# Kernel tuning notes

Hardware: AMD Instinct MI355X
Metric: run time of the kernel (lower is better)

Reference implementation:

```python
import jax, jax.numpy as jnp
import numpy as np
from jax.scipy.linalg import expm

D = 512      # d_model
S = 3        # num_scales
BATCH = 256
H = 8        # attention heads
HD = D // H  # head dim


def layernorm(x, g, b, eps=1e-5):
    m = jnp.mean(x, axis=-1, keepdims=True)
    v = jnp.var(x, axis=-1, keepdims=True)
    return (x - m) / jnp.sqrt(v + eps) * g + b


def setup_inputs() -> dict:
    key = jax.random.key(0)
    ks = jax.random.split(key, 16)
    sd = 1.0 / np.sqrt(D)
    inp = {
        'x': jax.random.normal(ks[0], (BATCH, D), jnp.float32),
        'h_prev': jax.random.normal(ks[1], (BATCH, D), jnp.float32),
        'lstm_h': jax.random.normal(ks[2], (S, BATCH, D), jnp.float32) * 0.1,
        'lstm_c': jax.random.normal(ks[3], (S, BATCH, D), jnp.float32) * 0.1,
        'A': jax.random.normal(ks[4], (D, D), jnp.float32) * sd,
        'Bm': jax.random.normal(ks[5], (D, D), jnp.float32) * sd,
        'dn_w1': jax.random.normal(ks[6], (D, D), jnp.float32) * sd,
        'dn_b1': jnp.zeros((D,), jnp.float32),
        'dn_g': jnp.ones((D,), jnp.float32),
        'dn_beta': jnp.zeros((D,), jnp.float32),
        'dn_w2': jax.random.normal(ks[7], (1, D), jnp.float32) * sd,
        'dn_b2': jnp.zeros((1,), jnp.float32),
        'lstm_wih': jax.random.normal(ks[8], (S, 4 * D, D), jnp.float32) * sd,
        'lstm_whh': jax.random.normal(ks[9], (S, 4 * D, D), jnp.float32) * sd,
        'lstm_bih': jnp.zeros((S, 4 * D), jnp.float32),
        'lstm_bhh': jnp.zeros((S, 4 * D), jnp.float32),
        'decays': jnp.linspace(0.5, 0.95, S, dtype=jnp.float32),
        'attn_in_w': jax.random.normal(ks[10], (3 * D, D), jnp.float32) * sd,
        'attn_in_b': jnp.zeros((3 * D,), jnp.float32),
        'attn_out_w': jax.random.normal(ks[11], (D, D), jnp.float32) * sd,
        'attn_out_b': jnp.zeros((D,), jnp.float32),
        'proj_w': jax.random.normal(ks[12], (D, (S + 2) * D), jnp.float32) * (1.0 / np.sqrt((S + 2) * D)),
        'proj_b': jnp.zeros((D,), jnp.float32),
        'proj_g': jnp.ones((D,), jnp.float32),
        'proj_beta': jnp.zeros((D,), jnp.float32),
    }
    return inp


def reference(x, h_prev, lstm_h, lstm_c, A, Bm, dn_w1, dn_b1, dn_g, dn_beta,
              dn_w2, dn_b2, lstm_wih, lstm_whh, lstm_bih, lstm_bhh, decays,
              attn_in_w, attn_in_b, attn_out_w, attn_out_b,
              proj_w, proj_b, proj_g, proj_beta):
    # ---- delta_net: Linear -> LayerNorm -> GELU(exact) -> Linear -> Softplus ----
    h1 = layernorm(x @ dn_w1.T + dn_b1, dn_g, dn_beta)
    h1 = jax.nn.gelu(h1, approximate=False)
    delta = jax.nn.softplus(h1 @ dn_w2.T + dn_b2)           # (B, 1)

    # ---- SSM update: h_t = expm(delta*A) h_prev + delta*B x ----
    A_disc = jax.vmap(expm)(delta[:, :, None] * A)          # (B, D, D)
    h_ssm = jnp.einsum('bij,bj->bi', A_disc, h_prev) + delta * jnp.einsum('ij,bj->bi', Bm, x)

    # ---- multi-scale LSTM cells (vectorized over scales) ----
    gates = (jnp.einsum('bd,skd->sbk', x, lstm_wih)
             + jnp.einsum('sbd,skd->sbk', lstm_h, lstm_whh)
             + (lstm_bih + lstm_bhh)[:, None, :])           # (S, B, 4D)
    gi, gf, gg, go = jnp.split(gates, 4, axis=-1)
    i_g = jax.nn.sigmoid(gi)
    f_g = jax.nn.sigmoid(gf)
    g_g = jnp.tanh(gg)
    o_g = jax.nn.sigmoid(go)
    c_raw = f_g * lstm_c + i_g * g_g                        # (S, B, D)
    h_new = o_g * jnp.tanh(c_raw)                           # (S, B, D)
    dec = decays[:, None, None]
    c_new = dec * lstm_c + (1.0 - dec) * c_raw              # (S, B, D)

    # ---- fusion attention: 1 query (h_ssm), S keys/values (h_new) ----
    Wq, Wk, Wv = jnp.split(attn_in_w, 3, axis=0)
    bq, bk, bv = jnp.split(attn_in_b, 3, axis=0)
    kv = jnp.transpose(h_new, (1, 0, 2))                    # (B, S, D)
    q = (h_ssm @ Wq.T + bq).reshape(-1, 1, H, HD).transpose(0, 2, 1, 3)   # (B,H,1,HD)
    k = (kv @ Wk.T + bk).reshape(-1, S, H, HD).transpose(0, 2, 1, 3)      # (B,H,S,HD)
    v = (kv @ Wv.T + bv).reshape(-1, S, H, HD).transpose(0, 2, 1, 3)
    scores = jnp.einsum('bhqe,bhke->bhqk', q, k) / np.sqrt(HD)
    attn = jax.nn.softmax(scores, axis=-1)
    ctx = jnp.einsum('bhqk,bhke->bhqe', attn, v)            # (B,H,1,HD)
    ctx = ctx.transpose(0, 2, 1, 3).reshape(-1, D)          # (B, D)
    fused = ctx @ attn_out_w.T + attn_out_b                 # (B, D)

    # ---- output projection over concat [h_ssm, fused, h_1..h_S] ----
    combined = jnp.concatenate([h_ssm, fused] + [h_new[i] for i in range(S)], axis=-1)
    output = layernorm(combined @ proj_w.T + proj_b, proj_g, proj_beta)
    return (output, h_ssm, h_new, c_new)
```

## Files before the change

### kernel.cpp

```cpp
#include <hip/hip_runtime.h>
#include <math.h>

#define DIM 512
#define NB 256
#define KMAX 12

using bf16x8 = __attribute__((ext_vector_type(8))) short;
using f32x4  = __attribute__((ext_vector_type(4))) float;
using float4v = __attribute__((ext_vector_type(4))) float;
using ushort4v = __attribute__((ext_vector_type(4))) unsigned short;

__device__ __forceinline__ unsigned short f2b(float f) {
    union { float f; unsigned int u; } v; v.f = f;
    unsigned int r = v.u + 0x7fffu + ((v.u >> 16) & 1u);
    return (unsigned short)(r >> 16);
}
__device__ __forceinline__ float b2f(unsigned short u) {
    union { unsigned int u; float f; } v; v.u = ((unsigned int)u) << 16;
    return v.f;
}
__device__ __forceinline__ ushort4v f2b4(float4v v) {
    ushort4v o;
    o.x = f2b(v.x); o.y = f2b(v.y); o.z = f2b(v.z); o.w = f2b(v.w);
    return o;
}

__device__ __forceinline__ void block_reduce2(float& s, float& q, float* sb1, float* sb2)
{
    int tid = threadIdx.x;
    #pragma unroll
    for (int off = 32; off > 0; off >>= 1) {
        s += __shfl_down(s, off);
        q += __shfl_down(q, off);
    }
    if ((tid & 63) == 0) { sb1[tid >> 6] = s; sb2[tid >> 6] = q; }
    __syncthreads();
    s = sb1[0] + sb1[1] + sb1[2] + sb1[3];
    q = sb2[0] + sb2[1] + sb2[2] + sb2[3];
    __syncthreads();
}

struct GemmDesc {
    const unsigned short* X;
    const unsigned short* W;
    const float* bias;
    float* Cf;
    unsigned short* Cb;
    unsigned short* Ct;
    int M, N, K, ldX, ldW, ldC, tr_row0, acc;
};
struct GemmArgs { GemmDesc d[10]; };
struct LnParams {
    const float* pre; const float* g; const float* beta;
    const float* w2; const float* b2; float* delta; float* coeff;
    int lnd_y;
};

__global__ __launch_bounds__(256) void gemm_mfma(GemmArgs args, LnParams lp)
{
    __shared__ unsigned short lsA[2][8192];
    __shared__ unsigned short lsB[2][8192];
    __shared__ float sb1[4], sb2[4];

    if ((int)blockIdx.y == lp.lnd_y) {
        int b = blockIdx.x, tid = threadIdx.x;
        int i0 = tid, i1 = tid + 256;
        float x0 = lp.pre[(size_t)b * DIM + i0];
        float x1 = lp.pre[(size_t)b * DIM + i1];
        float s = x0 + x1, q = x0 * x0 + x1 * x1;
        block_reduce2(s, q, sb1, sb2);
        float mean = s * (1.f / DIM);
        float var  = q * (1.f / DIM) - mean * mean;
        float inv  = rsqrtf(var + 1e-5f);
        float y0 = (x0 - mean) * inv * lp.g[i0] + lp.beta[i0];
        float y1 = (x1 - mean) * inv * lp.g[i1] + lp.beta[i1];
        float h0 = 0.5f * y0 * (1.f + erff(y0 * 0.70710678118654752f));
        float h1 = 0.5f * y1 * (1.f + erff(y1 * 0.70710678118654752f));
        float p = h0 * lp.w2[i0] + h1 * lp.w2[i1];
        float dummy = 0.f;
        block_reduce2(p, dummy, sb1, sb2);
        if (tid == 0) {
            float z = p + lp.b2[0];
            float d = (z > 20.f) ? z : log1pf(expf(z));
            lp.delta[b] = d;
            float c = 1.f;
            lp.coeff[b] = 1.f;
            for (int k = 1; k <= KMAX; ++k) { c *= d / (float)k; lp.coeff[k * 256 + b] = c; }
        }
        return;
    }

    GemmDesc de = args.d[blockIdx.y];
    int tn = de.N >> 6;
    int tiles = (de.M >> 6) * tn;
    int t = blockIdx.x;
    if (t >= tiles) return;
    int m0 = (t / tn) << 6;
    int n0 = (t % tn) << 6;

    int tid = threadIdx.x;
    int w = tid >> 6;
    int l = tid & 63;
    int nkt = de.K >> 7;

    int srow = w * 16 + (l >> 2);
    int schk = l & 3;
    const unsigned short* gA = de.X + (size_t)(m0 + srow) * de.ldX + schk * 8;
    const unsigned short* gB = de.W + (size_t)(n0 + srow) * de.ldW + schk * 8;
    unsigned short* lA = &lsA[0][(w * 64 + l) * 8];
    unsigned short* lB = &lsB[0][(w * 64 + l) * 8];

#define STAGE(bufi, kt)                                                          \
    do {                                                                         \
        for (int hh = 0; hh < 4; ++hh) {                                         \
            __builtin_amdgcn_global_load_lds(                                    \
                (const __attribute__((address_space(1))) unsigned int*)(gA + (size_t)(kt) * 128 + hh * 32), \
                (__attribute__((address_space(3))) unsigned int*)(lA + (bufi) * 8192 + hh * 2048), 16, 0, 0); \
            __builtin_amdgcn_global_load_lds(                                    \
                (const __attribute__((address_space(1))) unsigned int*)(gB + (size_t)(kt) * 128 + hh * 32), \
                (__attribute__((address_space(3))) unsigned int*)(lB + (bufi) * 8192 + hh * 2048), 16, 0, 0); \
        }                                                                        \
    } while (0)

    int mbase = (w >> 1) * 32;
    int nbase = (w & 1) * 32;

    f32x4 acc[2][2];
    #pragma unroll
    for (int i = 0; i < 2; ++i)
        #pragma unroll
        for (int j = 0; j < 2; ++j)
            acc[i][j] = (f32x4){0.f, 0.f, 0.f, 0.f};

    int kg = l >> 4;
    int fr = l & 15;
    int aslot = (mbase * 4 + fr * 4 + kg) * 8;
    int bslot = (nbase * 4 + fr * 4 + kg) * 8;

    STAGE(0, 0);

    for (int kt = 0; kt < nkt; ++kt) {
        __syncthreads();
        if (kt + 1 < nkt) STAGE((kt + 1) & 1, kt + 1);

        const unsigned short* bufA = &lsA[kt & 1][0];
        const unsigned short* bufB = &lsB[kt & 1][0];
        #pragma unroll
        for (int h = 0; h < 4; ++h) {
            bf16x8 a0 = *(const bf16x8*)(bufA + h * 2048 + aslot);
            bf16x8 a1 = *(const bf16x8*)(bufA + h * 2048 + aslot + 512);
            bf16x8 b0 = *(const bf16x8*)(bufB + h * 2048 + bslot);
            bf16x8 b1 = *(const bf16x8*)(bufB + h * 2048 + bslot + 512);
            acc[0][0] = __builtin_amdgcn_mfma_f32_16x16x32_bf16(a0, b0, acc[0][0], 0, 0, 0);
            acc[0][1] = __builtin_amdgcn_mfma_f32_16x16x32_bf16(a0, b1, acc[0][1], 0, 0, 0);
            acc[1][0] = __builtin_amdgcn_mfma_f32_16x16x32_bf16(a1, b0, acc[1][0], 0, 0, 0);
            acc[1][1] = __builtin_amdgcn_mfma_f32_16x16x32_bf16(a1, b1, acc[1][1], 0, 0, 0);
        }
    }

    #pragma unroll
    for (int mi = 0; mi < 2; ++mi) {
        #pragma unroll
        for (int ni = 0; ni < 2; ++ni) {
            int col = n0 + nbase + ni * 16 + fr;
            float bv = de.bias ? de.bias[col] : 0.f;
            #pragma unroll
            for (int r = 0; r < 4; ++r) {
                int row = m0 + mbase + mi * 16 + (l >> 4) * 4 + r;
                float v = acc[mi][ni][r] + bv;
                if (de.Cf) {
                    if (de.acc == 2)      atomicAdd(&de.Cf[(size_t)row * de.ldC + col], v);
                    else if (de.acc == 1) de.Cf[(size_t)row * de.ldC + col] += v;
                    else                  de.Cf[(size_t)row * de.ldC + col] = v;
                } else {
                    de.Cb[(size_t)row * de.ldC + col] = f2b(v);
                }
                if (de.Ct && row >= de.tr_row0)
                    de.Ct[(size_t)col * 512 + (row - de.tr_row0)] = f2b(v);
            }
        }
    }
#undef STAGE
}

#define NSEG 14
struct PrepArgs {
    const float* sA[NSEG]; const float* sB[NSEG]; unsigned short* dst[NSEG];
    int n4[NSEG], dRL4[NSEG], sRLA4[NSEG], sRLB4[NSEG], half4[NSEG], offA[NSEG];
    const float* A; unsigned short* ATb;
    float* gates_zero; int gz_n4;
};
__global__ __launch_bounds__(256) void prep_kernel(PrepArgs a)
{
    __shared__ float tile[32][33];
    int bid = blockIdx.x, tid = threadIdx.x;
    if (bid < 2048) {
        const int gstride = 2048 * 256;
        int g0 = bid * 256 + tid;
        for (int seg = 0; seg < NSEG; ++seg) {
            int n4 = a.n4[seg];
            const float* sA = a.sA[seg];
            const float* sB = a.sB[seg];
            unsigned short* d = a.dst[seg];
            int dRL4 = a.dRL4[seg], sRLA4 = a.sRLA4[seg], sRLB4 = a.sRLB4[seg];
            int half4 = a.half4[seg], offA = a.offA[seg];
            for (int i = g0; i < n4; i += gstride) {
                int r = i / dRL4, c = i - r * dRL4;
                const float* src = (c < half4)
                    ? sA + ((size_t)r * sRLA4 + offA + c) * 4
                    : sB + ((size_t)r * sRLB4 + (c - half4)) * 4;
                float4v v = *(const float4v*)src;
                *(ushort4v*)(d + (size_t)i * 4) = f2b4(v);
            }
        }
    } else if (bid < 2304) {
        int tt = bid - 2048;
        int bx = tt & 15, by = tt >> 4;
        int tx = tid & 31, ty = tid >> 5;
        #pragma unroll
        for (int i = 0; i < 32; i += 8)
            tile[ty + i][tx] = a.A[(size_t)(by * 32 + ty + i) * 512 + bx * 32 + tx];
        __syncthreads();
        #pragma unroll
        for (int i = 0; i < 32; i += 8)
            a.ATb[(size_t)(bx * 32 + ty + i) * 512 + by * 32 + tx] = f2b(tile[tx][ty + i]);
    } else {
        float4v* gz = (float4v*)a.gates_zero;
        int g0 = (bid - 2304) * 256 + tid;
        const int gstride = 128 * 256;
        float4v z = (float4v){0.f, 0.f, 0.f, 0.f};
        for (int i = g0; i < a.gz_n4; i += gstride) gz[i] = z;
    }
}

__global__ void pointwise_fused(
    const float* __restrict__ Tm, const float* __restrict__ coeff,
    const float* __restrict__ h_prev, const float* __restrict__ delta,
    const float* __restrict__ Bx, float* __restrict__ hssm,
    unsigned short* __restrict__ combb,
    const float* __restrict__ gates, const float* __restrict__ bih,
    const float* __restrict__ bhh, const float* __restrict__ cin,
    const float* __restrict__ decays,
    float* __restrict__ hout, float* __restrict__ cout,
    const float* __restrict__ proj_b, float* __restrict__ projout)
{
    int idx4 = blockIdx.x * 256 + threadIdx.x;
    int base = idx4 * 4;
    if (base < 131072) {
        int b = base >> 9, i = base & 511;
        const float* Tr = Tm + (size_t)b * (KMAX * DIM) + i;
        float4v a = *(const float4v*)(h_prev + base);
        #pragma unroll
        for (int k = 1; k <= KMAX; ++k) {
            float c = coeff[k * 256 + b];
            float4v t = *(const float4v*)(Tr + (size_t)(k - 1) * DIM);
            a.x += c * t.x; a.y += c * t.y; a.z += c * t.z; a.w += c * t.w;
        }
        float dl = delta[b];
        float4v bx = *(const float4v*)(Bx + base);
        a.x += dl * bx.x; a.y += dl * bx.y; a.z += dl * bx.z; a.w += dl * bx.w;
        *(float4v*)(hssm + base) = a;
        *(ushort4v*)(combb + (size_t)b * 2048 + i) = f2b4(a);
    } else if (base < 524288) {
        int i2 = base - 131072;
        int s = i2 / (NB * DIM);
        int r = i2 - s * (NB * DIM);
        int b = r >> 9, d = r & 511;
        const float* gr = gates + (size_t)s * 524288 + (size_t)b * 2048 + d;
        const float* bi = bih + s * 2048 + d;
        const float* bh = bhh + s * 2048 + d;
        float4v gi = *(const float4v*)(gr);
        float4v gf = *(const float4v*)(gr + 512);
        float4v gg = *(const float4v*)(gr + 1024);
        float4v go = *(const float4v*)(gr + 1536);
        float4v bi0 = *(const float4v*)(bi),        bh0 = *(const float4v*)(bh);
        float4v bi1 = *(const float4v*)(bi + 512),  bh1 = *(const float4v*)(bh + 512);
        float4v bi2 = *(const float4v*)(bi + 1024), bh2 = *(const float4v*)(bh + 1024);
        float4v bi3 = *(const float4v*)(bi + 1536), bh3 = *(const float4v*)(bh + 1536);
        float4v c = *(const float4v*)(cin + i2);
        float dec = decays[s];
        float4v hn, cn;
        #pragma unroll
        for (int j = 0; j < 4; ++j) {
            float vgi = ((const float*)&gi)[j] + ((const float*)&bi0)[j] + ((const float*)&bh0)[j];
            float vgf = ((const float*)&gf)[j] + ((const float*)&bi1)[j] + ((const float*)&bh1)[j];
            float vgg = ((const float*)&gg)[j] + ((const float*)&bi2)[j] + ((const float*)&bh2)[j];
            float vgo = ((const float*)&go)[j] + ((const float*)&bi3)[j] + ((const float*)&bh3)[j];
            float ig = 1.f / (1.f + expf(-vgi));
            float fg = 1.f / (1.f + expf(-vgf));
            float g_ = tanhf(vgg);
            float og = 1.f / (1.f + expf(-vgo));
            float cc = ((const float*)&c)[j];
            float craw = fg * cc + ig * g_;
            ((float*)&hn)[j] = og * tanhf(craw);
            ((float*)&cn)[j] = dec * cc + (1.f - dec) * craw;
        }
        *(float4v*)(hout + i2) = hn;
        *(float4v*)(cout + i2) = cn;
        *(ushort4v*)(combb + (size_t)b * 2048 + 512 + s * 512 + d) = f2b4(hn);
    } else {
        int i = idx4 - 131072;
        int c4 = i & 127;
        float4v pb = *(const float4v*)(proj_b + c4 * 4);
        *(float4v*)(projout + (size_t)i * 4) = pb;
    }
}

__global__ __launch_bounds__(256) void tail_kernel(
    const unsigned short* __restrict__ qb, const unsigned short* __restrict__ kvb,
    const unsigned short* __restrict__ aout_wb, const float* __restrict__ aout_b,
    const unsigned short* __restrict__ P2b, const float* __restrict__ projA,
    const float* __restrict__ fin_g, const float* __restrict__ fin_beta,
    float* __restrict__ outp)
{
    __shared__ float ctxs[512];
    __shared__ float fusedl[512];
    __shared__ float totals[512];
    __shared__ float sb1[4], sb2[4];
    int b = blockIdx.x, tid = threadIdx.x;

    if (tid < 128) {
        int h = tid >> 4, sub = (tid & 15) * 4;
        int col = h * 64 + sub;
        ushort4v q4 = *(const ushort4v*)(qb + (size_t)b * 512 + col);
        float qf[4] = { b2f(q4.x), b2f(q4.y), b2f(q4.z), b2f(q4.w) };
        float p[3];
        ushort4v k4[3], v4[3];
        #pragma unroll
        for (int s = 0; s < 3; ++s) {
            k4[s] = *(const ushort4v*)(kvb + (size_t)s * 262144 + (size_t)b * 1024 + col);
            v4[s] = *(const ushort4v*)(kvb + (size_t)s * 262144 + (size_t)b * 1024 + 512 + col);
            p[s] = qf[0] * b2f(k4[s].x) + qf[1] * b2f(k4[s].y)
                 + qf[2] * b2f(k4[s].z) + qf[3] * b2f(k4[s].w);
        }
        #pragma unroll
        for (int off = 1; off < 16; off <<= 1) {
            p[0] += __shfl_xor(p[0], off);
            p[1] += __shfl_xor(p[1], off);
            p[2] += __shfl_xor(p[2], off);
        }
        const float scale = 0.125f;
        float p0 = p[0] * scale, p1 = p[1] * scale, p2 = p[2] * scale;
        float m = fmaxf(p0, fmaxf(p1, p2));
        float w0 = expf(p0 - m), w1 = expf(p1 - m), w2 = expf(p2 - m);
        float invs = 1.f / (w0 + w1 + w2);
        ctxs[col + 0] = (w0 * b2f(v4[0].x) + w1 * b2f(v4[1].x) + w2 * b2f(v4[2].x)) * invs;
        ctxs[col + 1] = (w0 * b2f(v4[0].y) + w1 * b2f(v4[1].y) + w2 * b2f(v4[2].y)) * invs;
        ctxs[col + 2] = (w0 * b2f(v4[0].z) + w1 * b2f(v4[1].z) + w2 * b2f(v4[2].z)) * invs;
        ctxs[col + 3] = (w0 * b2f(v4[0].w) + w1 * b2f(v4[1].w) + w2 * b2f(v4[2].w)) * invs;
    }
    __syncthreads();

    for (int jj = tid; jj < 512; jj += 256) {
        float acc = aout_b[jj];
        const unsigned short* wr = aout_wb + (size_t)jj * 512;
        for (int k = 0; k < 512; k += 8) {
            ushort4v w0 = *(const ushort4v*)(wr + k);
            ushort4v w1 = *(const ushort4v*)(wr + k + 4);
            acc += ctxs[k+0]*b2f(w0.x) + ctxs[k+1]*b2f(w0.y)
                 + ctxs[k+2]*b2f(w0.z) + ctxs[k+3]*b2f(w0.w)
                 + ctxs[k+4]*b2f(w1.x) + ctxs[k+5]*b2f(w1.y)
                 + ctxs[k+6]*b2f(w1.z) + ctxs[k+7]*b2f(w1.w);
        }
        fusedl[jj] = acc;
    }
    __syncthreads();

    for (int ii = tid; ii < 512; ii += 256) {
        float acc = projA[(size_t)b * 512 + ii];
        const unsigned short* pr = P2b + (size_t)ii * 512;
        for (int j = 0; j < 512; j += 8) {
            ushort4v w0 = *(const ushort4v*)(pr + j);
            ushort4v w1 = *(const ushort4v*)(pr + j + 4);
            acc += fusedl[j+0]*b2f(w0.x) + fusedl[j+1]*b2f(w0.y)
                 + fusedl[j+2]*b2f(w0.z) + fusedl[j+3]*b2f(w0.w)
                 + fusedl[j+4]*b2f(w1.x) + fusedl[j+5]*b2f(w1.y)
                 + fusedl[j+6]*b2f(w1.z) + fusedl[j+7]*b2f(w1.w);
        }
        totals[ii] = acc;
    }
    __syncthreads();

    float x0 = totals[tid], x1 = totals[tid + 256];
    float s = x0 + x1, q = x0 * x0 + x1 * x1;
    block_reduce2(s, q, sb1, sb2);
    float mean = s * (1.f / DIM);
    float var  = q * (1.f / DIM) - mean * mean;
    float inv  = rsqrtf(var + 1e-5f);
    outp[(size_t)b * DIM + tid]       = (x0 - mean) * inv * fin_g[tid]       + fin_beta[tid];
    outp[(size_t)b * DIM + tid + 256] = (x1 - mean) * inv * fin_g[tid + 256] + fin_beta[tid + 256];
}

extern "C" void kernel_launch(void* const* d_in, const int* in_sizes, int n_in,
                              void* d_out, int out_size, void* d_ws, size_t ws_size,
                              hipStream_t stream)
{
    const float* x        = (const float*)d_in[0];
    const float* h_prev   = (const float*)d_in[1];
    const float* lstm_h   = (const float*)d_in[2];
    const float* lstm_c   = (const float*)d_in[3];
    const float* A        = (const float*)d_in[4];
    const float* Bm       = (const float*)d_in[5];
    const float* dn_w1    = (const float*)d_in[6];
    const float* dn_b1    = (const float*)d_in[7];
    const float* dn_g     = (const float*)d_in[8];
    const float* dn_beta  = (const float*)d_in[9];
    const float* dn_w2    = (const float*)d_in[10];
    const float* dn_b2    = (const float*)d_in[11];
    const float* wih      = (const float*)d_in[12];
    const float* whh      = (const float*)d_in[13];
    const float* bih      = (const float*)d_in[14];
    const float* bhh      = (const float*)d_in[15];
    const float* decays   = (const float*)d_in[16];
    const float* ain_w    = (const float*)d_in[17];
    const float* ain_b    = (const float*)d_in[18];
    const float* aout_w   = (const float*)d_in[19];
    const float* aout_b   = (const float*)d_in[20];
    const float* proj_w   = (const float*)d_in[21];
    const float* proj_b   = (const float*)d_in[22];
    const float* proj_g   = (const float*)d_in[23];
    const float* proj_bt  = (const float*)d_in[24];

    float* out  = (float*)d_out;
    float* hssm = out + 131072;
    float* hnew = out + 262144;
    float* cnew = out + 655360;

    unsigned short* us = (unsigned short*)d_ws;
    unsigned short* hpb     = us;
    unsigned short* ATb     = us + 131072;
    unsigned short* dn_w1b  = us + 393216;
    unsigned short* Bmb     = us + 655360;
    unsigned short* ain_wb  = us + 917504;
    unsigned short* proj_wb = us + 1703936;
    unsigned short* P2b     = us + 2752512;
    unsigned short* aout_wb = us + 3014656;
    unsigned short* Pw      = us + 3276800;
    unsigned short* Qa      = us + 5373952;
    unsigned short* Qb      = us + 5636096;
    unsigned short* Wcat    = us + 5898240;
    unsigned short* Xcat    = us + 12189696;
    unsigned short* combb   = us + 12976128;
    unsigned short* qb      = us + 13500416;
    unsigned short* kvb     = us + 13631488;
    unsigned short* U8b     = us + 14417920;
    float* fbase  = (float*)(us + 14548992);
    float* pre1   = fbase;
    float* delta  = fbase + 131072;
    float* coeff  = fbase + 131328;
    float* Bx     = fbase + 134656;
    float* Tm     = fbase + 265728;
    float* gates  = fbase + 1838592;
    float* projout = pre1;

    LnParams lpOff; lpOff.pre = nullptr; lpOff.g = nullptr; lpOff.beta = nullptr;
    lpOff.w2 = nullptr; lpOff.b2 = nullptr; lpOff.delta = nullptr; lpOff.coeff = nullptr;
    lpOff.lnd_y = -1;

    PrepArgs pa;
    int sidx = 0;
    auto LIN = [&](const float* s, unsigned short* d, int n4) {
        pa.sA[sidx]=s; pa.sB[sidx]=s; pa.dst[sidx]=d; pa.n4[sidx]=n4;
        pa.dRL4[sidx]=n4; pa.sRLA4[sidx]=0; pa.sRLB4[sidx]=0;
        pa.half4[sidx]=n4; pa.offA[sidx]=0; ++sidx;
    };
    LIN(h_prev, hpb,     32768);
    LIN(A,      Pw,      65536);
    LIN(dn_w1,  dn_w1b,  65536);
    LIN(Bm,     Bmb,     65536);
    LIN(ain_w,  ain_wb,  196608);
    LIN(aout_w, aout_wb, 65536);
    pa.sA[sidx]=proj_w; pa.sB[sidx]=proj_w + 1024; pa.dst[sidx]=proj_wb; pa.n4[sidx]=262144;
    pa.dRL4[sidx]=512; pa.sRLA4[sidx]=640; pa.sRLB4[sidx]=640; pa.half4[sidx]=128; pa.offA[sidx]=0; ++sidx;
    pa.sA[sidx]=proj_w; pa.sB[sidx]=proj_w; pa.dst[sidx]=P2b; pa.n4[sidx]=65536;
    pa.dRL4[sidx]=128; pa.sRLA4[sidx]=640; pa.sRLB4[sidx]=640; pa.half4[sidx]=128; pa.offA[sidx]=128; ++sidx;
    for (int s = 0; s < 3; ++s) {
        pa.sA[sidx]=wih + (size_t)s*1048576; pa.sB[sidx]=whh + (size_t)s*1048576;
        pa.dst[sidx]=Wcat + (size_t)s*2097152; pa.n4[sidx]=524288;
        pa.dRL4[sidx]=256; pa.sRLA4[sidx]=128; pa.sRLB4[sidx]=128; pa.half4[sidx]=128; pa.offA[sidx]=0; ++sidx;
    }
    for (int s = 0; s < 3; ++s) {
        pa.sA[sidx]=x; pa.sB[sidx]=lstm_h + (size_t)s*131072;
        pa.dst[sidx]=Xcat + (size_t)s*262144; pa.n4[sidx]=65536;
        pa.dRL4[sidx]=256; pa.sRLA4[sidx]=128; pa.sRLB4[sidx]=128; pa.half4[sidx]=128; pa.offA[sidx]=0; ++sidx;
    }
    pa.A = A; pa.ATb = ATb;
    pa.gates_zero = gates; pa.gz_n4 = 393216;
    prep_kernel<<<2432, 256, 0, stream>>>(pa);

    GemmArgs ga;
    ga.d[0] = { Xcat, dn_w1b, dn_b1, pre1, nullptr, nullptr, 256, 512, 512, 1024, 512, 512, 0, 0 };
    ga.d[1] = { Xcat, Bmb,    nullptr, Bx,  nullptr, nullptr, 256, 512, 512, 1024, 512, 512, 0, 0 };
    ga.d[2] = { Pw, ATb, nullptr, nullptr, Pw + 1*262144, Qa, 512, 512, 512, 512, 512, 512, 0, 0 };
    for (int s = 0; s < 3; ++s)
        for (int half = 0; half < 2; ++half)
            ga.d[3 + s * 2 + half] = { Xcat + (size_t)s * 262144 + half * 512,
                                       Wcat + (size_t)s * 2097152 + half * 512, nullptr,
                                       gates + (size_t)s * 524288, nullptr, nullptr,
                                       256, 2048, 512, 1024, 1024, 2048, 0, 2 };
    gemm_mfma<<<dim3(128, 9), 256, 0, stream>>>(ga, lpOff);

    LnParams lp1 = { pre1, dn_g, dn_beta, dn_w2, dn_b2, delta, coeff, 1 };
    ga.d[0] = { Pw, Qa, nullptr, nullptr, Pw + 2*262144, Qb, 1024, 512, 512, 512, 512, 512, 512, 0 };
    gemm_mfma<<<dim3(256, 2), 256, 0, stream>>>(ga, lp1);

    ga.d[0] = { Pw, Qb, nullptr, nullptr, Pw + 4*262144, nullptr, 2048, 512, 512, 512, 512, 512, 0, 0 };
    gemm_mfma<<<dim3(256, 1), 256, 0, stream>>>(ga, lpOff);

    ga.d[0] = { hpb, Pw, nullptr, Tm, nullptr, nullptr, 256, 4096, 512, 512, 512, 6144, 0, 0 };
    ga.d[1] = { hpb, Pw + 7*262144, nullptr, nullptr, U8b, nullptr, 256, 512, 512, 512, 512, 512, 0, 0 };
    gemm_mfma<<<dim3(256, 2), 256, 0, stream>>>(ga, lpOff);

    ga.d[0] = { U8b, Pw, nullptr, Tm + 4096, nullptr, nullptr, 256, 2048, 512, 512, 512, 6144, 0, 0 };
    gemm_mfma<<<dim3(128, 1), 256, 0, stream>>>(ga, lpOff);

    pointwise_fused<<<640, 256, 0, stream>>>(Tm, coeff, h_prev, delta, Bx, hssm, combb,
                                             gates, bih, bhh, lstm_c, decays, hnew, cnew,
                                             proj_b, projout);

    ga.d[0] = { combb, ain_wb, ain_b, nullptr, qb, nullptr, 256, 512, 512, 2048, 512, 512, 0, 0 };
    for (int s = 0; s < 3; ++s)
        ga.d[1 + s] = { combb + 512 + (size_t)s * 512, ain_wb + 262144, ain_b + 512,
                        nullptr, kvb + (size_t)s * 262144, nullptr, 256, 1024, 512, 2048, 512, 1024, 0, 0 };
    for (int ks = 0; ks < 4; ++ks)
        ga.d[4 + ks] = { combb + ks * 512, proj_wb + ks * 512, nullptr, projout, nullptr, nullptr,
                         256, 512, 512, 2048, 2048, 512, 0, 2 };
    gemm_mfma<<<dim3(64, 8), 256, 0, stream>>>(ga, lpOff);

    tail_kernel<<<256, 256, 0, stream>>>(qb, kvb, aout_wb, aout_b, P2b, projout,
                                         proj_g, proj_bt, out);
}
```

Measured before the change: 232.1 us.

## Fold attention out-projection into output projection and drop split-K atomics

```diff
diff --git a/kernel.cpp b/kernel.cpp
--- a/kernel.cpp
+++ b/kernel.cpp
@@ -183,12 +183,12 @@
 #undef STAGE
 }
 
-#define NSEG 14
+#define NSEG 13
 struct PrepArgs {
     const float* sA[NSEG]; const float* sB[NSEG]; unsigned short* dst[NSEG];
     int n4[NSEG], dRL4[NSEG], sRLA4[NSEG], sRLB4[NSEG], half4[NSEG], offA[NSEG];
     const float* A; unsigned short* ATb;
-    float* gates_zero; int gz_n4;
+    const float* W2src; unsigned short* W2dst;
 };
 __global__ __launch_bounds__(256) void prep_kernel(PrepArgs a)
 {
@@ -213,23 +213,20 @@
                 *(ushort4v*)(d + (size_t)i * 4) = f2b4(v);
             }
         }
-    } else if (bid < 2304) {
+    } else {
         int tt = bid - 2048;
+        const float* src = a.A;
+        unsigned short* dst = a.ATb;
+        if (tt >= 256) { tt -= 256; src = a.W2src; dst = a.W2dst; }
         int bx = tt & 15, by = tt >> 4;
         int tx = tid & 31, ty = tid >> 5;
         #pragma unroll
         for (int i = 0; i < 32; i += 8)
-            tile[ty + i][tx] = a.A[(size_t)(by * 32 + ty + i) * 512 + bx * 32 + tx];
+            tile[ty + i][tx] = src[(size_t)(by * 32 + ty + i) * 512 + bx * 32 + tx];
         __syncthreads();
         #pragma unroll
         for (int i = 0; i < 32; i += 8)
-            a.ATb[(size_t)(bx * 32 + ty + i) * 512 + by * 32 + tx] = f2b(tile[tx][ty + i]);
-    } else {
-        float4v* gz = (float4v*)a.gates_zero;
-        int g0 = (bid - 2304) * 256 + tid;
-        const int gstride = 128 * 256;
-        float4v z = (float4v){0.f, 0.f, 0.f, 0.f};
-        for (int i = g0; i < a.gz_n4; i += gstride) gz[i] = z;
+            dst[(size_t)(bx * 32 + ty + i) * 512 + by * 32 + tx] = f2b(tile[tx][ty + i]);
     }
 }
 
@@ -242,7 +239,8 @@
     const float* __restrict__ bhh, const float* __restrict__ cin,
     const float* __restrict__ decays,
     float* __restrict__ hout, float* __restrict__ cout,
-    const float* __restrict__ proj_b, float* __restrict__ projout)
+    const unsigned short* __restrict__ P2b, const float* __restrict__ aout_b,
+    const float* __restrict__ proj_b, float* __restrict__ pbc)
 {
     int idx4 = blockIdx.x * 256 + threadIdx.x;
     int base = idx4 * 4;
@@ -299,23 +297,30 @@
         *(float4v*)(cout + i2) = cn;
         *(ushort4v*)(combb + (size_t)b * 2048 + 512 + s * 512 + d) = f2b4(hn);
     } else {
-        int i = idx4 - 131072;
-        int c4 = i & 127;
-        float4v pb = *(const float4v*)(proj_b + c4 * 4);
-        *(float4v*)(projout + (size_t)i * 4) = pb;
+        int ii = idx4 - 131072;
+        const unsigned short* pr = P2b + (size_t)ii * 512;
+        float acc = 0.f;
+        for (int k = 0; k < 512; k += 8) {
+            ushort4v w0 = *(const ushort4v*)(pr + k);
+            ushort4v w1 = *(const ushort4v*)(pr + k + 4);
+            float4v a0 = *(const float4v*)(aout_b + k);
+            float4v a1 = *(const float4v*)(aout_b + k + 4);
+            acc += a0.x * b2f(w0.x) + a0.y * b2f(w0.y)
+                 + a0.z * b2f(w0.z) + a0.w * b2f(w0.w)
+                 + a1.x * b2f(w1.x) + a1.y * b2f(w1.y)
+                 + a1.z * b2f(w1.z) + a1.w * b2f(w1.w);
+        }
+        pbc[ii] = proj_b[ii] + acc;
     }
 }
 
 __global__ __launch_bounds__(256) void tail_kernel(
     const unsigned short* __restrict__ qb, const unsigned short* __restrict__ kvb,
-    const unsigned short* __restrict__ aout_wb, const float* __restrict__ aout_b,
-    const unsigned short* __restrict__ P2b, const float* __restrict__ projA,
+    const unsigned short* __restrict__ M2b, const float* __restrict__ projA,
     const float* __restrict__ fin_g, const float* __restrict__ fin_beta,
     float* __restrict__ outp)
 {
     __shared__ float ctxs[512];
-    __shared__ float fusedl[512];
-    __shared__ float totals[512];
     __shared__ float sb1[4], sb2[4];
     int b = blockIdx.x, tid = threadIdx.x;
 
@@ -351,37 +356,25 @@
     }
     __syncthreads();
 
-    for (int jj = tid; jj < 512; jj += 256) {
-        float acc = aout_b[jj];
-        const unsigned short* wr = aout_wb + (size_t)jj * 512;
+    float x0 = projA[(size_t)b * 512 + tid];
+    float x1 = projA[(size_t)b * 512 + tid + 256];
+    {
+        const unsigned short* mr0 = M2b + (size_t)tid * 512;
+        const unsigned short* mr1 = M2b + (size_t)(tid + 256) * 512;
         for (int k = 0; k < 512; k += 8) {
-            ushort4v w0 = *(const ushort4v*)(wr + k);
-            ushort4v w1 = *(const ushort4v*)(wr + k + 4);
-            acc += ctxs[k+0]*b2f(w0.x) + ctxs[k+1]*b2f(w0.y)
-                 + ctxs[k+2]*b2f(w0.z) + ctxs[k+3]*b2f(w0.w)
-                 + ctxs[k+4]*b2f(w1.x) + ctxs[k+5]*b2f(w1.y)
-                 + ctxs[k+6]*b2f(w1.z) + ctxs[k+7]*b2f(w1.w);
-        }
-        fusedl[jj] = acc;
-    }
-    __syncthreads();
-
-    for (int ii = tid; ii < 512; ii += 256) {
-        float acc = projA[(size_t)b * 512 + ii];
-        const unsigned short* pr = P2b + (size_t)ii * 512;
-        for (int j = 0; j < 512; j += 8) {
-            ushort4v w0 = *(const ushort4v*)(pr + j);
-            ushort4v w1 = *(const ushort4v*)(pr + j + 4);
-            acc += fusedl[j+0]*b2f(w0.x) + fusedl[j+1]*b2f(w0.y)
-                 + fusedl[j+2]*b2f(w0.z) + fusedl[j+3]*b2f(w0.w)
-                 + fusedl[j+4]*b2f(w1.x) + fusedl[j+5]*b2f(w1.y)
-                 + fusedl[j+6]*b2f(w1.z) + fusedl[j+7]*b2f(w1.w);
-        }
-        totals[ii] = acc;
-    }
-    __syncthreads();
-
-    float x0 = totals[tid], x1 = totals[tid + 256];
+            ushort4v a0 = *(const ushort4v*)(mr0 + k);
+            ushort4v a1 = *(const ushort4v*)(mr0 + k + 4);
+            ushort4v c0 = *(const ushort4v*)(mr1 + k);
+            ushort4v c1 = *(const ushort4v*)(mr1 + k + 4);
+            float t0 = ctxs[k+0], t1 = ctxs[k+1], t2 = ctxs[k+2], t3 = ctxs[k+3];
+            float t4 = ctxs[k+4], t5 = ctxs[k+5], t6 = ctxs[k+6], t7 = ctxs[k+7];
+            x0 += t0*b2f(a0.x) + t1*b2f(a0.y) + t2*b2f(a0.z) + t3*b2f(a0.w)
+                + t4*b2f(a1.x) + t5*b2f(a1.y) + t6*b2f(a1.z) + t7*b2f(a1.w);
+            x1 += t0*b2f(c0.x) + t1*b2f(c0.y) + t2*b2f(c0.z) + t3*b2f(c0.w)
+                + t4*b2f(c1.x) + t5*b2f(c1.y) + t6*b2f(c1.z) + t7*b2f(c1.w);
+        }
+    }
+
     float s = x0 + x1, q = x0 * x0 + x1 * x1;
     block_reduce2(s, q, sb1, sb2);
     float mean = s * (1.f / DIM);
@@ -434,7 +427,7 @@
     unsigned short* ain_wb  = us + 917504;
     unsigned short* proj_wb = us + 1703936;
     unsigned short* P2b     = us + 2752512;
-    unsigned short* aout_wb = us + 3014656;
+    unsigned short* aout_wTb= us + 3014656;
     unsigned short* Pw      = us + 3276800;
     unsigned short* Qa      = us + 5373952;
     unsigned short* Qb      = us + 5636096;
@@ -451,6 +444,8 @@
     float* Bx     = fbase + 134656;
     float* Tm     = fbase + 265728;
     float* gates  = fbase + 1838592;
+    float* pbc    = fbase + 3411456;
+    unsigned short* M2b = (unsigned short*)(fbase + 3412480);
     float* projout = pre1;
 
     LnParams lpOff; lpOff.pre = nullptr; lpOff.g = nullptr; lpOff.beta = nullptr;
@@ -469,7 +464,6 @@
     LIN(dn_w1,  dn_w1b,  65536);
     LIN(Bm,     Bmb,     65536);
     LIN(ain_w,  ain_wb,  196608);
-    LIN(aout_w, aout_wb, 65536);
     pa.sA[sidx]=proj_w; pa.sB[sidx]=proj_w + 1024; pa.dst[sidx]=proj_wb; pa.n4[sidx]=262144;
     pa.dRL4[sidx]=512; pa.sRLA4[sidx]=640; pa.sRLB4[sidx]=640; pa.half4[sidx]=128; pa.offA[sidx]=0; ++sidx;
     pa.sA[sidx]=proj_w; pa.sB[sidx]=proj_w; pa.dst[sidx]=P2b; pa.n4[sidx]=65536;
@@ -485,20 +479,19 @@
         pa.dRL4[sidx]=256; pa.sRLA4[sidx]=128; pa.sRLB4[sidx]=128; pa.half4[sidx]=128; pa.offA[sidx]=0; ++sidx;
     }
     pa.A = A; pa.ATb = ATb;
-    pa.gates_zero = gates; pa.gz_n4 = 393216;
-    prep_kernel<<<2432, 256, 0, stream>>>(pa);
+    pa.W2src = aout_w; pa.W2dst = aout_wTb;
+    prep_kernel<<<2560, 256, 0, stream>>>(pa);
 
     GemmArgs ga;
     ga.d[0] = { Xcat, dn_w1b, dn_b1, pre1, nullptr, nullptr, 256, 512, 512, 1024, 512, 512, 0, 0 };
     ga.d[1] = { Xcat, Bmb,    nullptr, Bx,  nullptr, nullptr, 256, 512, 512, 1024, 512, 512, 0, 0 };
     ga.d[2] = { Pw, ATb, nullptr, nullptr, Pw + 1*262144, Qa, 512, 512, 512, 512, 512, 512, 0, 0 };
     for (int s = 0; s < 3; ++s)
-        for (int half = 0; half < 2; ++half)
-            ga.d[3 + s * 2 + half] = { Xcat + (size_t)s * 262144 + half * 512,
-                                       Wcat + (size_t)s * 2097152 + half * 512, nullptr,
-                                       gates + (size_t)s * 524288, nullptr, nullptr,
-                                       256, 2048, 512, 1024, 1024, 2048, 0, 2 };
-    gemm_mfma<<<dim3(128, 9), 256, 0, stream>>>(ga, lpOff);
+        ga.d[3 + s] = { Xcat + (size_t)s * 262144, Wcat + (size_t)s * 2097152, nullptr,
+                        gates + (size_t)s * 524288, nullptr, nullptr,
+                        256, 2048, 1024, 1024, 1024, 2048, 0, 0 };
+    ga.d[6] = { P2b, aout_wTb, nullptr, nullptr, M2b, nullptr, 512, 512, 512, 512, 512, 512, 0, 0 };
+    gemm_mfma<<<dim3(128, 7), 256, 0, stream>>>(ga, lpOff);
 
     LnParams lp1 = { pre1, dn_g, dn_beta, dn_w2, dn_b2, delta, coeff, 1 };
     ga.d[0] = { Pw, Qa, nullptr, nullptr, Pw + 2*262144, Qb, 1024, 512, 512, 512, 512, 512, 512, 0 };
@@ -514,19 +507,17 @@
     ga.d[0] = { U8b, Pw, nullptr, Tm + 4096, nullptr, nullptr, 256, 2048, 512, 512, 512, 6144, 0, 0 };
     gemm_mfma<<<dim3(128, 1), 256, 0, stream>>>(ga, lpOff);
 
-    pointwise_fused<<<640, 256, 0, stream>>>(Tm, coeff, h_prev, delta, Bx, hssm, combb,
+    pointwise_fused<<<514, 256, 0, stream>>>(Tm, coeff, h_prev, delta, Bx, hssm, combb,
                                              gates, bih, bhh, lstm_c, decays, hnew, cnew,
-                                             proj_b, projout);
+                                             P2b, aout_b, proj_b, pbc);
 
     ga.d[0] = { combb, ain_wb, ain_b, nullptr, qb, nullptr, 256, 512, 512, 2048, 512, 512, 0, 0 };
     for (int s = 0; s < 3; ++s)
         ga.d[1 + s] = { combb + 512 + (size_t)s * 512, ain_wb + 262144, ain_b + 512,
                         nullptr, kvb + (size_t)s * 262144, nullptr, 256, 1024, 512, 2048, 512, 1024, 0, 0 };
-    for (int ks = 0; ks < 4; ++ks)
-        ga.d[4 + ks] = { combb + ks * 512, proj_wb + ks * 512, nullptr, projout, nullptr, nullptr,
-                         256, 512, 512, 2048, 2048, 512, 0, 2 };
-    gemm_mfma<<<dim3(64, 8), 256, 0, stream>>>(ga, lpOff);
-
-    tail_kernel<<<256, 256, 0, stream>>>(qb, kvb, aout_wb, aout_b, P2b, projout,
+    ga.d[4] = { combb, proj_wb, pbc, projout, nullptr, nullptr, 256, 512, 2048, 2048, 2048, 512, 0, 0 };
+    gemm_mfma<<<dim3(64, 5), 256, 0, stream>>>(ga, lpOff);
+
+    tail_kernel<<<256, 256, 0, stream>>>(qb, kvb, M2b, projout,
                                          proj_g, proj_bt, out);
 }
```

Measured after the change: 230.3 us. Within noise of the previous version (-0.8%).
